# Kernel tuning notes

Measured on AMD Instinct MI355X. Metric: run time of the kernel, lower is better.

The kernel has to match this reference:

```python
import jax, jax.numpy as jnp
import numpy as np

N_CLASS = 85
BLANK = N_CLASS - 1  # blank_index = n_class - 1
ALPHA = 0.05
B, T, D = 4096, 96, 64


def setup_inputs() -> dict:
    key = jax.random.key(0)
    k1, k2, k3, k4 = jax.random.split(key, 4)
    preds = jax.random.normal(k1, (B, T, N_CLASS), dtype=jnp.float32)
    features = jax.random.normal(k2, (B, T, D), dtype=jnp.float32)
    labels = jax.random.randint(k3, (B, T), 0, N_CLASS, dtype=jnp.int32)
    centers = jax.random.normal(k4, (N_CLASS, D), dtype=jnp.float32) * 0.01
    return {"preds": preds, "features": features, "labels": labels, "centers": centers}


def _char_mask(pred_labels):
    # CTC collapse: keep non-blank positions that are the last of a repeat run.
    is_char = pred_labels != BLANK
    rep = pred_labels[:, :-1] == pred_labels[:, 1:]          # [B, T-1]
    tail = pred_labels[:, :1] > BLANK                         # always False (as in source)
    char_rep = jnp.concatenate([rep, tail], axis=1)           # [B, T]
    return is_char & jnp.logical_not(char_rep)


def reference(preds, features, labels, centers):
    # preds:    [B, T, n_class] softmax/logits -> argmax decode
    # features: [B, T, feat_dims]
    # labels:   [B, T] int, char label aligned to each timestep
    pred_labels = jnp.argmax(preds, axis=-1)                  # [B, T]
    mask = _char_mask(pred_labels).astype(features.dtype)     # [B, T] ragged-as-mask

    centers_batch = centers[labels]                           # gather -> [B, T, D]
    diff = centers_batch - features                           # [B, T, D]

    # tf.nn.l2_loss = sum(x^2)/2, restricted to valid char positions
    loss = 0.5 * jnp.sum(mask * jnp.sum(diff * diff, axis=-1))

    # unique_with_counts analog: per-class counts of valid char positions
    labels_flat = labels.reshape(-1)
    mask_flat = mask.reshape(-1)
    counts = jax.ops.segment_sum(mask_flat, labels_flat, num_segments=N_CLASS)  # [n_class]
    appear = counts[labels]                                   # [B, T]

    # alpha * diff / (1 + appear_times), zeroed outside char positions
    delta = ALPHA * diff * (mask / (1.0 + appear))[..., None]  # [B, T, D]

    # scatter_nd: centers.assign_sub(scatter of per-char deltas)
    upd = jax.ops.segment_sum(delta.reshape(-1, D), labels_flat, num_segments=N_CLASS)
    new_centers = centers - upd                               # [n_class, D]
    return loss, new_centers
```

## Files before the change

kernel.cpp:

```cpp
#include <hip/hip_runtime.h>
#include <cstdint>

#define BB     4096
#define TT     96
#define NC     85
#define BLANKC 84
#define DD     64
#define ALPHA  0.05f
#define BT     (BB * TT)
#define SLICE_F (NC * 17)
#define NF4    (TT * NC / 4)

__global__ __launch_bounds__(512) void k_amask(const float4* __restrict__ p4,
                                               const int* __restrict__ labels,
                                               unsigned* __restrict__ labm,
                                               int* __restrict__ hpartT,
                                               float* __restrict__ out) {
    __shared__ float rows[TT * NC];
    __shared__ int   pls[TT];
    __shared__ int   h[NC];
    int tid  = threadIdx.x;
    int b    = blockIdx.x;
    int lane = tid & 63;
    int w    = tid >> 6;
    if (tid < NC) h[tid] = 0;
    if (b == 0 && tid == 480) out[0] = 0.f;
    int labreg = (tid < TT) ? labels[b * TT + tid] : 0;

    {
        const float4* src = p4 + (size_t)b * NF4 + 255 * w;
        float4* dst = (float4*)(rows + (size_t)w * 12 * NC);
        float4 v0 = src[lane];
        float4 v1 = src[lane + 64];
        float4 v2 = src[lane + 128];
        float4 v3 = (lane < 63) ? src[lane + 192] : v2;
        dst[lane]       = v0;
        dst[lane + 64]  = v1;
        dst[lane + 128] = v2;
        if (lane < 63) dst[lane + 192] = v3;
    }
    {
        const int c0t[4] = {0, 22, 43, 64};
        const int c1t[4] = {22, 43, 64, 85};
        int r  = lane >> 2;
        int q  = lane & 3;
        float bv = -3.4e38f; int bc = 127;
        if (lane < 48) {
            const float* row = rows + (w * 12 + r) * NC;
            int c0 = c0t[q], c1 = c1t[q];
            bv = row[c0]; bc = c0;
            for (int c = c0 + 1; c < c1; ++c) {
                float v = row[c];
                if (v > bv) { bv = v; bc = c; }
            }
        }
#pragma unroll
        for (int m = 1; m <= 2; m <<= 1) {
            float ov = __shfl_xor(bv, m);
            int   oc = __shfl_xor(bc, m);
            if (ov > bv || (ov == bv && oc < bc)) { bv = ov; bc = oc; }
        }
        if (lane < 48 && (lane & 3) == 0) pls[w * 12 + r] = bc;
    }
    __syncthreads();
    if (tid < TT) {
        int p = pls[tid];
        int m = (p != BLANKC) && (tid == TT - 1 || p != pls[tid + 1]);
        labm[b * TT + tid] = (unsigned)labreg | ((unsigned)m << 31);
        atomicAdd(&h[labreg], m);
    }
    __syncthreads();
    if (tid < NC) hpartT[tid * BB + b] = h[tid];
}

__global__ __launch_bounds__(512, 6) void k_main(const float* __restrict__ feat,
                                                 const unsigned* __restrict__ labm,
                                                 float* __restrict__ updp,
                                                 float* __restrict__ lossp, int nb) {
    __shared__ float sl[8 * SLICE_F];
    __shared__ float lred[8];
    int tid = threadIdx.x;
    for (int i = tid; i < 8 * SLICE_F; i += 512) sl[i] = 0.f;
    __syncthreads();

    int lane = tid & 63;
    int w    = tid >> 6;
    int dq   = w & 3;
    int wg   = w >> 2;
    int sub  = lane >> 4;
    int l16  = lane & 15;
    float* slice = sl + w * SLICE_F;

    int ppc = BT / (nb * 2);
    int p0  = (blockIdx.x * 2 + wg) * ppc;
    int nss = ppc / 16;
    const float* fbase = feat + dq * 16 + l16;

    float lsum = 0.f;
    float fA0, fA1, fA2, fA3, fB0, fB1, fB2, fB3;
    uint4 lA0, lA1, lA2, lA3, lB0, lB1, lB2, lB3;

#define ISSUE(P, f0, f1, f2, f3, q0, q1, q2, q3) do {            \
    int _p = (P);                                                \
    q0 = *(const uint4*)(labm + _p);                             \
    q1 = *(const uint4*)(labm + _p + 4);                         \
    q2 = *(const uint4*)(labm + _p + 8);                         \
    q3 = *(const uint4*)(labm + _p + 12);                        \
    f0 = fbase[(size_t)(_p + sub) * DD];                         \
    f1 = fbase[(size_t)(_p + 4 + sub) * DD];                     \
    f2 = fbase[(size_t)(_p + 8 + sub) * DD];                     \
    f3 = fbase[(size_t)(_p + 12 + sub) * DD];                    \
} while (0)

#define SUBSTEP(lv, fc) do {                                     \
    unsigned a0 = lv.x & 0x7fffffffu, a1 = lv.y & 0x7fffffffu,   \
             a2 = lv.z & 0x7fffffffu, a3 = lv.w & 0x7fffffffu;   \
    bool dup = (a0 == a1) | (a0 == a2) | (a0 == a3) |            \
               (a1 == a2) | (a1 == a3) | (a2 == a3);             \
    unsigned lw = (sub & 2) ? ((sub & 1) ? lv.w : lv.z)          \
                            : ((sub & 1) ? lv.y : lv.x);         \
    float m = (float)(lw >> 31);                                 \
    int  la = (int)(lw & 0x7fffffffu);                           \
    float c = m * (fc);                                          \
    lsum = fmaf(c, (fc), lsum);                                  \
    int a = la * 17 + l16;                                       \
    if (!dup) slice[a] += c;                                     \
    else      atomicAdd(&slice[a], c);                           \
} while (0)

    ISSUE(p0, fA0, fA1, fA2, fA3, lA0, lA1, lA2, lA3);
    for (int ss = 0; ss < nss; ss += 2) {
        if (ss + 1 < nss)
            ISSUE(p0 + (ss + 1) * 16, fB0, fB1, fB2, fB3, lB0, lB1, lB2, lB3);
        SUBSTEP(lA0, fA0); SUBSTEP(lA1, fA1);
        SUBSTEP(lA2, fA2); SUBSTEP(lA3, fA3);
        if (ss + 1 < nss) {
            if (ss + 2 < nss)
                ISSUE(p0 + (ss + 2) * 16, fA0, fA1, fA2, fA3, lA0, lA1, lA2, lA3);
            SUBSTEP(lB0, fB0); SUBSTEP(lB1, fB1);
            SUBSTEP(lB2, fB2); SUBSTEP(lB3, fB3);
        }
    }
#undef ISSUE
#undef SUBSTEP
    __syncthreads();

    float* myp = updp + (size_t)blockIdx.x * (NC * DD);
    for (int i = tid; i < NC * DD; i += 512) {
        int r = i >> 6, d = i & 63;
        int qq = d >> 4, d16 = d & 15;
        myp[i] = sl[qq * SLICE_F + r * 17 + d16] +
                 sl[(qq + 4) * SLICE_F + r * 17 + d16];
    }
#pragma unroll
    for (int off = 32; off; off >>= 1) lsum += __shfl_xor(lsum, off);
    if (lane == 0) lred[w] = lsum;
    __syncthreads();
    if (tid == 0) {
        float s = 0.f;
#pragma unroll
        for (int ww = 0; ww < 8; ++ww) s += lred[ww];
        lossp[blockIdx.x] = s;
    }
}

__global__ __launch_bounds__(256) void k_reduce(const float* __restrict__ updp,
                                                const float* __restrict__ lossp,
                                                const float* __restrict__ centers,
                                                const int* __restrict__ hpartT,
                                                float* __restrict__ out, int nb) {
    __shared__ float sred[256];
    __shared__ float sr[4];
    __shared__ int   scnt;
    int tid = threadIdx.x;
    int bid = blockIdx.x;
    if (bid < NC * 4) {
        int j = bid >> 2, q = bid & 3;
        int cs = 0;
        for (int t = tid; t < BB; t += 256) cs += hpartT[j * BB + t];
#pragma unroll
        for (int off = 32; off; off >>= 1) cs += __shfl_xor(cs, off);
        int lane = tid & 63, wv = tid >> 6;
        if (lane == 0) ((int*)sred)[wv] = cs;
        __syncthreads();
        if (tid == 0)
            scnt = ((int*)sred)[0] + ((int*)sred)[1] +
                   ((int*)sred)[2] + ((int*)sred)[3];
        __syncthreads();
        float cnt = (float)scnt;
        int i = tid & 15;
        int c16 = tid >> 4;
        int per = nb >> 4;
        int col = j * DD + q * 16 + i;
        float s = 0.f;
        for (int b = c16 * per; b < (c16 + 1) * per; ++b)
            s += updp[(size_t)b * (NC * DD) + col];
        sred[tid] = s;
        __syncthreads();
        if (tid < 16) {
            float F = 0.f;
#pragma unroll
            for (int cc = 0; cc < 16; ++cc) F += sred[cc * 16 + i];
            float c   = centers[col];
            float scale = ALPHA / (1.f + cnt);
            out[1 + col] = c - scale * (cnt * c - F);
            float lp = cnt * c * c - 2.f * c * F;
#pragma unroll
            for (int off = 8; off; off >>= 1) lp += __shfl_xor(lp, off);
            if (i == 0) atomicAdd(&out[0], 0.5f * lp);
        }
    } else {
        float s = 0.f;
        for (int t = tid; t < nb; t += 256) s += lossp[t];
#pragma unroll
        for (int off = 32; off; off >>= 1) s += __shfl_xor(s, off);
        int lane = tid & 63, wv = tid >> 6;
        if (lane == 0) sr[wv] = s;
        __syncthreads();
        if (tid == 0) atomicAdd(&out[0], 0.5f * (sr[0] + sr[1] + sr[2] + sr[3]));
    }
}

extern "C" void kernel_launch(void* const* d_in, const int* in_sizes, int n_in,
                              void* d_out, int out_size, void* d_ws, size_t ws_size,
                              hipStream_t stream) {
    const float* preds    = (const float*)d_in[0];
    const float* features = (const float*)d_in[1];
    const int*   labels   = (const int*)d_in[2];
    const float* centers  = (const float*)d_in[3];
    float* out = (float*)d_out;

    char* ws = (char*)d_ws;
    unsigned* labm = (unsigned*)ws;
    int* hpartT    = (int*)(ws + 4 * (size_t)BT);
    size_t off0 = 4 * (size_t)BT + (size_t)NC * BB * 4 + 512;

    int nb = 768;
    while (nb > 16 && off0 + (size_t)nb * 4 + 512 +
                      (size_t)nb * NC * DD * 4 > ws_size)
        nb >>= 1;
    float* lossp = (float*)(ws + off0);
    float* updp  = (float*)(ws + off0 + (size_t)nb * 4 + 512);

    k_amask<<<BB, 512, 0, stream>>>((const float4*)preds, labels, labm,
                                    hpartT, out);
    k_main<<<nb, 512, 0, stream>>>(features, labm, updp, lossp, nb);
    k_reduce<<<NC * 4 + 1, 256, 0, stream>>>(updp, lossp, centers, hpartT,
                                             out, nb);
}
```

Measured before the change: 85.42 us.

## Process four batch rows per argmax block with register prefetch; fix main grid size

The argmax/mask kernel now handles four batch rows per block instead of one. While the current row's argmax is computed from shared memory, the next row's preds are loaded into registers. This cuts the block count and the per-block histogram partials by 4x, which also shrinks the count reduction in k_reduce. The main kernel's grid is now a compile-time 512 blocks instead of a runtime-chosen 768, so the partial-update reduction sees fewer partials, at the cost of less parallelism in k_main and less latency hiding in k_amask.

After: 82.70 us. 3.2% less time.

```diff
diff --git a/kernel.cpp b/kernel.cpp
--- a/kernel.cpp
+++ b/kernel.cpp
@@ -10,43 +10,52 @@
 #define BT     (BB * TT)
 #define SLICE_F (NC * 17)
 #define NF4    (TT * NC / 4)
+#define RPBA   4
+#define NBA    (BB / RPBA)
+#define NBM    512
 
 __global__ __launch_bounds__(512) void k_amask(const float4* __restrict__ p4,
                                                const int* __restrict__ labels,
                                                unsigned* __restrict__ labm,
                                                int* __restrict__ hpartT,
                                                float* __restrict__ out) {
-    __shared__ float rows[TT * NC];
-    __shared__ int   pls[TT];
+    __shared__ float rows[8][12 * NC];
+    __shared__ int   pls[RPBA * TT + 1];
     __shared__ int   h[NC];
     int tid  = threadIdx.x;
-    int b    = blockIdx.x;
+    int blk  = blockIdx.x;
     int lane = tid & 63;
     int w    = tid >> 6;
     if (tid < NC) h[tid] = 0;
-    if (b == 0 && tid == 480) out[0] = 0.f;
-    int labreg = (tid < TT) ? labels[b * TT + tid] : 0;
-
-    {
-        const float4* src = p4 + (size_t)b * NF4 + 255 * w;
-        float4* dst = (float4*)(rows + (size_t)w * 12 * NC);
-        float4 v0 = src[lane];
-        float4 v1 = src[lane + 64];
-        float4 v2 = src[lane + 128];
-        float4 v3 = (lane < 63) ? src[lane + 192] : v2;
+    if (blk == 0 && tid == 480) out[0] = 0.f;
+    int labreg = (tid < RPBA * TT) ? labels[blk * RPBA * TT + tid] : 0;
+
+    const float4* src = p4 + (size_t)(blk * RPBA) * NF4 + 255 * w;
+    float4 v0 = src[lane];
+    float4 v1 = src[lane + 64];
+    float4 v2 = src[lane + 128];
+    float4 v3 = src[min(lane + 192, 254)];
+
+    const int c0t[4] = {0, 22, 43, 64};
+    const int c1t[4] = {22, 43, 64, 85};
+
+    for (int i = 0; i < RPBA; ++i) {
+        float4* dst = (float4*)rows[w];
         dst[lane]       = v0;
         dst[lane + 64]  = v1;
         dst[lane + 128] = v2;
         if (lane < 63) dst[lane + 192] = v3;
-    }
-    {
-        const int c0t[4] = {0, 22, 43, 64};
-        const int c1t[4] = {22, 43, 64, 85};
-        int r  = lane >> 2;
-        int q  = lane & 3;
+        if (i + 1 < RPBA) {
+            const float4* s2 = p4 + (size_t)(blk * RPBA + i + 1) * NF4 + 255 * w;
+            v0 = s2[lane];
+            v1 = s2[lane + 64];
+            v2 = s2[lane + 128];
+            v3 = s2[min(lane + 192, 254)];
+        }
+        int r = lane >> 2, q = lane & 3;
         float bv = -3.4e38f; int bc = 127;
         if (lane < 48) {
-            const float* row = rows + (w * 12 + r) * NC;
+            const float* row = rows[w] + r * NC;
             int c0 = c0t[q], c1 = c1t[q];
             bv = row[c0]; bc = c0;
             for (int c = c0 + 1; c < c1; ++c) {
@@ -60,23 +69,24 @@
             int   oc = __shfl_xor(bc, m);
             if (ov > bv || (ov == bv && oc < bc)) { bv = ov; bc = oc; }
         }
-        if (lane < 48 && (lane & 3) == 0) pls[w * 12 + r] = bc;
-    }
-    __syncthreads();
-    if (tid < TT) {
-        int p = pls[tid];
-        int m = (p != BLANKC) && (tid == TT - 1 || p != pls[tid + 1]);
-        labm[b * TT + tid] = (unsigned)labreg | ((unsigned)m << 31);
+        if (lane < 48 && (lane & 3) == 0) pls[i * TT + w * 12 + r] = bc;
+    }
+    __syncthreads();
+    if (tid < RPBA * TT) {
+        int p  = pls[tid];
+        int lp = tid % TT;
+        int m  = (p != BLANKC) && (lp == TT - 1 || p != pls[tid + 1]);
+        labm[blk * RPBA * TT + tid] = (unsigned)labreg | ((unsigned)m << 31);
         atomicAdd(&h[labreg], m);
     }
     __syncthreads();
-    if (tid < NC) hpartT[tid * BB + b] = h[tid];
+    if (tid < NC) hpartT[tid * NBA + blk] = h[tid];
 }
 
 __global__ __launch_bounds__(512, 6) void k_main(const float* __restrict__ feat,
                                                  const unsigned* __restrict__ labm,
                                                  float* __restrict__ updp,
-                                                 float* __restrict__ lossp, int nb) {
+                                                 float* __restrict__ lossp) {
     __shared__ float sl[8 * SLICE_F];
     __shared__ float lred[8];
     int tid = threadIdx.x;
@@ -91,9 +101,9 @@
     int l16  = lane & 15;
     float* slice = sl + w * SLICE_F;
 
-    int ppc = BT / (nb * 2);
+    const int ppc = BT / (NBM * 2);
+    const int nss = ppc / 16;
     int p0  = (blockIdx.x * 2 + wg) * ppc;
-    int nss = ppc / 16;
     const float* fbase = feat + dq * 16 + l16;
 
     float lsum = 0.f;
@@ -168,7 +178,7 @@
                                                 const float* __restrict__ lossp,
                                                 const float* __restrict__ centers,
                                                 const int* __restrict__ hpartT,
-                                                float* __restrict__ out, int nb) {
+                                                float* __restrict__ out) {
     __shared__ float sred[256];
     __shared__ float sr[4];
     __shared__ int   scnt;
@@ -177,7 +187,7 @@
     if (bid < NC * 4) {
         int j = bid >> 2, q = bid & 3;
         int cs = 0;
-        for (int t = tid; t < BB; t += 256) cs += hpartT[j * BB + t];
+        for (int t = tid; t < NBA; t += 256) cs += hpartT[j * NBA + t];
 #pragma unroll
         for (int off = 32; off; off >>= 1) cs += __shfl_xor(cs, off);
         int lane = tid & 63, wv = tid >> 6;
@@ -190,7 +200,7 @@
         float cnt = (float)scnt;
         int i = tid & 15;
         int c16 = tid >> 4;
-        int per = nb >> 4;
+        const int per = NBM >> 4;
         int col = j * DD + q * 16 + i;
         float s = 0.f;
         for (int b = c16 * per; b < (c16 + 1) * per; ++b)
@@ -211,7 +221,7 @@
         }
     } else {
         float s = 0.f;
-        for (int t = tid; t < nb; t += 256) s += lossp[t];
+        for (int t = tid; t < NBM; t += 256) s += lossp[t];
 #pragma unroll
         for (int off = 32; off; off >>= 1) s += __shfl_xor(s, off);
         int lane = tid & 63, wv = tid >> 6;
@@ -233,18 +243,12 @@
     char* ws = (char*)d_ws;
     unsigned* labm = (unsigned*)ws;
     int* hpartT    = (int*)(ws + 4 * (size_t)BT);
-    size_t off0 = 4 * (size_t)BT + (size_t)NC * BB * 4 + 512;
-
-    int nb = 768;
-    while (nb > 16 && off0 + (size_t)nb * 4 + 512 +
-                      (size_t)nb * NC * DD * 4 > ws_size)
-        nb >>= 1;
+    size_t off0 = 4 * (size_t)BT + (size_t)NC * NBA * 4 + 512;
     float* lossp = (float*)(ws + off0);
-    float* updp  = (float*)(ws + off0 + (size_t)nb * 4 + 512);
-
-    k_amask<<<BB, 512, 0, stream>>>((const float4*)preds, labels, labm,
-                                    hpartT, out);
-    k_main<<<nb, 512, 0, stream>>>(features, labm, updp, lossp, nb);
-    k_reduce<<<NC * 4 + 1, 256, 0, stream>>>(updp, lossp, centers, hpartT,
-                                             out, nb);
-}
+    float* updp  = (float*)(ws + off0 + (size_t)NBM * 4 + 512);
+
+    k_amask<<<NBA, 512, 0, stream>>>((const float4*)preds, labels, labm,
+                                     hpartT, out);
+    k_main<<<NBM, 512, 0, stream>>>(features, labm, updp, lossp);
+    k_reduce<<<NC * 4 + 1, 256, 0, stream>>>(updp, lossp, centers, hpartT, out);
+}
```
